# Kernel optimization log

Measured on AMD Instinct MI355X. Metric: run time of the kernel, lower is better.

The kernel has to match this reference:

```python
import jax, jax.numpy as jnp
import numpy as np

N_NODES = 100000
N_EDGES = 1600000
IN_FEATS = 256
HEADS = 4
OUT_FEATS = 32


def setup_inputs() -> dict:
    key = jax.random.key(0)
    k1, k2, k3, k4, k5, k6 = jax.random.split(key, 6)
    feat = jax.random.normal(k1, (N_NODES, IN_FEATS), dtype=jnp.float32)
    fc_w = jax.random.normal(k2, (HEADS * OUT_FEATS, IN_FEATS), dtype=jnp.float32) * (1.0 / np.sqrt(IN_FEATS))
    attn_l = jax.random.normal(k3, (1, HEADS, OUT_FEATS), dtype=jnp.float32) * 0.1
    attn_r = jax.random.normal(k4, (1, HEADS, OUT_FEATS), dtype=jnp.float32) * 0.1
    src = jax.random.randint(k5, (N_EDGES,), 0, N_NODES, dtype=jnp.int32)
    dst = jax.random.randint(k6, (N_EDGES,), 0, N_NODES, dtype=jnp.int32)
    return {"feat": feat, "fc_w": fc_w, "attn_l": attn_l, "attn_r": attn_r, "src": src, "dst": dst}


def reference(feat, fc_w, attn_l, attn_r, src, dst):
    # feat: [N, F_in]; fc_w: [H*D, F_in]; attn_l/r: [1, H, D]; src/dst: [E]
    N = feat.shape[0]
    H, D = attn_l.shape[1], attn_l.shape[2]
    # linear projection (no bias), viewed as [N, H, D]
    ft = (feat @ fc_w.T).reshape(N, H, D)
    # per-node attention logits
    el = jnp.einsum('nhd,hd->nh', ft, attn_l[0])  # [N, H]
    er = jnp.einsum('nhd,hd->nh', ft, attn_r[0])  # [N, H]
    # per-edge score: leaky_relu(el[src] + er[dst])
    e = jax.nn.leaky_relu(el[src] + er[dst], negative_slope=0.2)  # [E, H]
    # edge softmax over incoming edges of each dst node (stable)
    emax = jax.ops.segment_max(e, dst, num_segments=N)  # [N, H]
    a = jnp.exp(e - emax[dst])  # [E, H]
    asum = jax.ops.segment_sum(a, dst, num_segments=N)  # [N, H]
    a = a / asum[dst]
    # attn_drop is a no-op in eval mode; weighted scatter-sum aggregation
    msg = ft[src] * a[:, :, None]  # [E, H, D]
    out = jax.ops.segment_sum(msg, dst, num_segments=N)  # [N, H, D]
    # final_layer=False, activation=None, norm=None -> flatten heads
    return out.reshape(N, H * D)
```

## Files before the change

kernel.cpp:

```cpp
#include <hip/hip_runtime.h>
#include <hip/hip_bf16.h>
#include <float.h>

#define IN_F 256
#define HD   128
#define NH   4
#define GM   128

typedef __bf16 bf16x8 __attribute__((ext_vector_type(8)));
typedef __bf16 bf16x2 __attribute__((ext_vector_type(2)));
typedef float  f32x4  __attribute__((ext_vector_type(4)));

__device__ __forceinline__ bf16x8 cvt8(const float4 a, const float4 b) {
    bf16x8 r;
    r[0] = (__bf16)a.x; r[1] = (__bf16)a.y; r[2] = (__bf16)a.z; r[3] = (__bf16)a.w;
    r[4] = (__bf16)b.x; r[5] = (__bf16)b.y; r[6] = (__bf16)b.z; r[7] = (__bf16)b.w;
    return r;
}

__global__ __launch_bounds__(256) void gemm_ft_mfma(const float* __restrict__ feat,
                                                    const float* __restrict__ w,
                                                    __bf16* __restrict__ ft,
                                                    int N, int ntiles) {
    __shared__ __align__(16) __bf16 Bs[128][264];
    __shared__ __align__(16) __bf16 As[GM][40];
    const int t = threadIdx.x;
    const int wv = t >> 6;
    const int lane = t & 63;

    {
        const int col = t >> 1;
        const int koff = (t & 1) * 128;
        const float* wp = w + (size_t)col * IN_F + koff;
#pragma unroll
        for (int i = 0; i < 128; i += 8) {
            const float4 v0 = *(const float4*)(wp + i);
            const float4 v1 = *(const float4*)(wp + i + 4);
            *(bf16x8*)&Bs[col][koff + i] = cvt8(v0, v1);
        }
    }

    const int ar = t >> 1;
    const int ac = (t & 1) * 16;
    const int frow = lane & 15;
    const int fk   = (lane >> 4) * 8;

    for (int tile = blockIdx.x; tile < ntiles; tile += gridDim.x) {
        const int row0 = tile * GM;
        f32x4 acc[2][8];
#pragma unroll
        for (int mt = 0; mt < 2; ++mt)
#pragma unroll
            for (int ct = 0; ct < 8; ++ct) acc[mt][ct] = {0.f, 0.f, 0.f, 0.f};

        for (int ks = 0; ks < 8; ++ks) {
            const int k0 = ks * 32;
            __syncthreads();
            bf16x8 av0, av1;
            const int gr = row0 + ar;
            if (gr < N) {
                const float* fp = feat + (size_t)gr * IN_F + k0 + ac;
                const float4 v0 = *(const float4*)(fp);
                const float4 v1 = *(const float4*)(fp + 4);
                const float4 v2 = *(const float4*)(fp + 8);
                const float4 v3 = *(const float4*)(fp + 12);
                av0 = cvt8(v0, v1);
                av1 = cvt8(v2, v3);
            } else {
#pragma unroll
                for (int i = 0; i < 8; ++i) { av0[i] = (__bf16)0.f; av1[i] = (__bf16)0.f; }
            }
            *(bf16x8*)&As[ar][ac] = av0;
            *(bf16x8*)&As[ar][ac + 8] = av1;
            __syncthreads();

            const bf16x8 af0 = *(const bf16x8*)&As[wv * 32 + frow][fk];
            const bf16x8 af1 = *(const bf16x8*)&As[wv * 32 + 16 + frow][fk];
#pragma unroll
            for (int ct = 0; ct < 8; ++ct) {
                const bf16x8 bfrag = *(const bf16x8*)&Bs[ct * 16 + frow][k0 + fk];
                acc[0][ct] = __builtin_amdgcn_mfma_f32_16x16x32_bf16(af0, bfrag, acc[0][ct], 0, 0, 0);
                acc[1][ct] = __builtin_amdgcn_mfma_f32_16x16x32_bf16(af1, bfrag, acc[1][ct], 0, 0, 0);
            }
        }
        const int rb = row0 + wv * 32 + (lane >> 4) * 4;
#pragma unroll
        for (int mt = 0; mt < 2; ++mt)
#pragma unroll
            for (int ct = 0; ct < 8; ++ct)
#pragma unroll
                for (int reg = 0; reg < 4; ++reg) {
                    const int m = rb + mt * 16 + reg;
                    if (m < N) ft[(size_t)m * HD + ct * 16 + frow] = (__bf16)acc[mt][ct][reg];
                }
    }
}

__global__ __launch_bounds__(256) void eler_k(const __bf16* __restrict__ ft,
                                              const float* __restrict__ attn_l,
                                              const float* __restrict__ attn_r,
                                              float* __restrict__ el,
                                              float* __restrict__ er, int N) {
    const int lane = threadIdx.x & 63;
    const int node = blockIdx.x * 4 + (threadIdx.x >> 6);
    if (node >= N) return;
    const bf16x2 f  = *(const bf16x2*)(ft + (size_t)node * HD + lane * 2);
    const float2 al = *(const float2*)(attn_l + lane * 2);
    const float2 ar = *(const float2*)(attn_r + lane * 2);
    const float fx = (float)f[0], fy = (float)f[1];
    float pl = fx * al.x + fy * al.y;
    float pr = fx * ar.x + fy * ar.y;
#pragma unroll
    for (int s = 1; s < 16; s <<= 1) {
        pl += __shfl_xor(pl, s);
        pr += __shfl_xor(pr, s);
    }
    if ((lane & 15) == 0) {
        const int h = lane >> 4;
        el[(size_t)node * NH + h] = pl;
        er[(size_t)node * NH + h] = pr;
    }
}

__global__ __launch_bounds__(256) void deg_rank_k(const int* __restrict__ dst,
                                                  int* __restrict__ deg,
                                                  int* __restrict__ rank, int E) {
    const int i = blockIdx.x * 256 + threadIdx.x;
    if (i < E) rank[i] = atomicAdd(&deg[dst[i]], 1);
}

__global__ __launch_bounds__(1024) void scan1_k(const int* __restrict__ deg,
                                                int* __restrict__ off,
                                                int* __restrict__ bsum, int N) {
    __shared__ int lds[1024];
    const int t = threadIdx.x;
    const int g = blockIdx.x * 1024 + t;
    const int x = (g < N) ? deg[g] : 0;
    lds[t] = x;
    __syncthreads();
    int v = x;
    for (int s = 1; s < 1024; s <<= 1) {
        const int add = (t >= s) ? lds[t - s] : 0;
        __syncthreads();
        v += add;
        lds[t] = v;
        __syncthreads();
    }
    if (g < N) off[g] = v - x;
    if (t == 1023) bsum[blockIdx.x] = v;
}

__global__ __launch_bounds__(128) void scan2_k(const int* __restrict__ bsum,
                                               int* __restrict__ boff, int nb) {
    __shared__ int lds[128];
    const int t = threadIdx.x;
    const int x = (t < nb) ? bsum[t] : 0;
    lds[t] = x;
    __syncthreads();
    int v = x;
    for (int s = 1; s < 128; s <<= 1) {
        const int add = (t >= s) ? lds[t - s] : 0;
        __syncthreads();
        v += add;
        lds[t] = v;
        __syncthreads();
    }
    boff[t] = v - x;
}

__global__ __launch_bounds__(256) void scatter_k(const int* __restrict__ src,
                                                 const int* __restrict__ dst,
                                                 const int* __restrict__ off,
                                                 const int* __restrict__ boff,
                                                 const int* __restrict__ rank,
                                                 int* __restrict__ ssrc, int E) {
    const int i = blockIdx.x * 256 + threadIdx.x;
    if (i < E) {
        const int d = dst[i];
        const int p = off[d] + boff[d >> 10] + rank[i];
        ssrc[p] = src[i];
    }
}

__global__ __launch_bounds__(64) void aggregate_k(const __bf16* __restrict__ ft,
                                                  const float* __restrict__ el,
                                                  const float* __restrict__ er,
                                                  const int* __restrict__ deg,
                                                  const int* __restrict__ off,
                                                  const int* __restrict__ boff,
                                                  const int* __restrict__ ssrc,
                                                  float* __restrict__ out, int N) {
    const int n = blockIdx.x;
    const int lane = threadIdx.x;
    const int il = lane & 15;
    const int q  = lane >> 4;
    const int h  = il >> 2;
    float4* outp = (float4*)(out + (size_t)n * HD);
    const int dn = deg[n];
    if (dn == 0) {
        if (q < 2) outp[il * 2 + q] = make_float4(0.f, 0.f, 0.f, 0.f);
        return;
    }
    const int start = off[n] + boff[n >> 10];
    const float4 er4 = *(const float4*)(er + (size_t)n * NH);

    __shared__ float a_lds[64 * NH];
    __shared__ int   s_lds[64];
    float4 ssum = make_float4(0.f, 0.f, 0.f, 0.f);
    float acc[8];
#pragma unroll
    for (int i = 0; i < 8; ++i) acc[i] = 0.f;

    for (int c0 = 0; c0 < dn; c0 += 64) {
        const int j = c0 + lane;
        float4 a = make_float4(0.f, 0.f, 0.f, 0.f);
        int sv = 0;
        if (j < dn) {
            sv = ssrc[start + j];
            float4 e = *(const float4*)(el + (size_t)sv * NH);
            e.x += er4.x; e.y += er4.y; e.z += er4.z; e.w += er4.w;
            e.x = e.x >= 0.f ? e.x : 0.2f * e.x;
            e.y = e.y >= 0.f ? e.y : 0.2f * e.y;
            e.z = e.z >= 0.f ? e.z : 0.2f * e.z;
            e.w = e.w >= 0.f ? e.w : 0.2f * e.w;
            a.x = __expf(e.x); a.y = __expf(e.y);
            a.z = __expf(e.z); a.w = __expf(e.w);
            ssum.x += a.x; ssum.y += a.y; ssum.z += a.z; ssum.w += a.w;
        }
        s_lds[lane] = sv;
        *(float4*)(a_lds + lane * NH) = a;
        __syncthreads();
        const int cnt = min(64, dn - c0);
        for (int j2 = 0; j2 < cnt; j2 += 8) {
            const int e0 = j2 + q;
            const int e1 = j2 + 4 + q;
            const int sv0 = s_lds[e0];
            const int sv1 = s_lds[e1];
            const float a0 = a_lds[e0 * NH + h];
            const float a1 = a_lds[e1 * NH + h];
            const bf16x8 f0 = *(const bf16x8*)(ft + (size_t)sv0 * HD + il * 8);
            const bf16x8 f1 = *(const bf16x8*)(ft + (size_t)sv1 * HD + il * 8);
#pragma unroll
            for (int k = 0; k < 8; ++k) acc[k] = fmaf(a0, (float)f0[k], acc[k]);
#pragma unroll
            for (int k = 0; k < 8; ++k) acc[k] = fmaf(a1, (float)f1[k], acc[k]);
        }
        __syncthreads();
    }
#pragma unroll
    for (int s = 1; s < 64; s <<= 1) {
        ssum.x += __shfl_xor(ssum.x, s);
        ssum.y += __shfl_xor(ssum.y, s);
        ssum.z += __shfl_xor(ssum.z, s);
        ssum.w += __shfl_xor(ssum.w, s);
    }
#pragma unroll
    for (int k = 0; k < 8; ++k) {
        acc[k] += __shfl_xor(acc[k], 16);
        acc[k] += __shfl_xor(acc[k], 32);
    }
    const float sumh = (h == 0) ? ssum.x : (h == 1) ? ssum.y : (h == 2) ? ssum.z : ssum.w;
    const float inv = 1.f / sumh;
    if (q < 2) {
        const int b = q * 4;
        outp[il * 2 + q] = make_float4(acc[b] * inv, acc[b + 1] * inv,
                                       acc[b + 2] * inv, acc[b + 3] * inv);
    }
}

extern "C" void kernel_launch(void* const* d_in, const int* in_sizes, int n_in,
                              void* d_out, int out_size, void* d_ws, size_t ws_size,
                              hipStream_t stream) {
    const float* feat   = (const float*)d_in[0];
    const float* fc_w   = (const float*)d_in[1];
    const float* attn_l = (const float*)d_in[2];
    const float* attn_r = (const float*)d_in[3];
    const int*   src    = (const int*)d_in[4];
    const int*   dst    = (const int*)d_in[5];
    const int N = in_sizes[0] / IN_F;
    const int E = in_sizes[4];
    float* out = (float*)d_out;

    char* wp = (char*)d_ws;
    __bf16* ft = (__bf16*)wp; wp += (size_t)N * HD * 2;
    float* el  = (float*)wp; wp += (size_t)N * NH * 4;
    float* er  = (float*)wp; wp += (size_t)N * NH * 4;
    int* deg   = (int*)wp;   wp += (size_t)N * 4;
    int* off   = (int*)wp;   wp += (size_t)N * 4;
    int* bsum  = (int*)wp;   wp += 1024;
    int* boff  = (int*)wp;   wp += 1024;
    int* rank  = (int*)wp;   wp += (size_t)E * 4;
    int* ssrc  = (int*)wp;   wp += (size_t)E * 4;

    hipMemsetAsync(deg, 0, (size_t)N * 4, stream);

    const int ntiles = (N + GM - 1) / GM;
    gemm_ft_mfma<<<dim3(512), dim3(256), 0, stream>>>(feat, fc_w, ft, N, ntiles);
    eler_k<<<dim3((N + 3) / 4), dim3(256), 0, stream>>>(ft, attn_l, attn_r, el, er, N);
    deg_rank_k<<<dim3((E + 255) / 256), dim3(256), 0, stream>>>(dst, deg, rank, E);
    const int nblk = (N + 1023) >> 10;
    scan1_k<<<dim3(nblk), dim3(1024), 0, stream>>>(deg, off, bsum, N);
    scan2_k<<<dim3(1), dim3(128), 0, stream>>>(bsum, boff, nblk);
    scatter_k<<<dim3((E + 255) / 256), dim3(256), 0, stream>>>(src, dst, off, boff, rank, ssrc, E);
    aggregate_k<<<dim3(N), dim3(64), 0, stream>>>(ft, el, er, deg, off, boff, ssrc, out, N);
}
```

Measured before the change: 386.9 us.

## Fuse el/er logits and degree counting into GEMM with register prefetch

Merges the projection GEMM, the per-node attention logit computation and the destination degree/rank atomic counting into one kernel, which removes two launches and the re-read of ft. el/er are now computed from the fp32 MFMA accumulators using cross-lane shuffles instead of from the bf16-rounded ft. The feat tile for the next k-step is also prefetched into registers so that global loads overlap the MFMA work. In exchange the kernel uses more registers and its GEMM phase is delayed by the atomic loop, and el/er now differ slightly numerically from the bf16 path.

```diff
diff --git a/kernel.cpp b/kernel.cpp
--- a/kernel.cpp
+++ b/kernel.cpp
@@ -18,10 +18,17 @@
     return r;
 }
 
-__global__ __launch_bounds__(256) void gemm_ft_mfma(const float* __restrict__ feat,
-                                                    const float* __restrict__ w,
-                                                    __bf16* __restrict__ ft,
-                                                    int N, int ntiles) {
+__global__ __launch_bounds__(256) void gemm_fused(const float* __restrict__ feat,
+                                                  const float* __restrict__ w,
+                                                  const float* __restrict__ attn_l,
+                                                  const float* __restrict__ attn_r,
+                                                  const int* __restrict__ dst,
+                                                  __bf16* __restrict__ ft,
+                                                  float* __restrict__ el,
+                                                  float* __restrict__ er,
+                                                  int* __restrict__ deg,
+                                                  int* __restrict__ rank,
+                                                  int N, int E, int ntiles) {
     __shared__ __align__(16) __bf16 Bs[128][264];
     __shared__ __align__(16) __bf16 As[GM][40];
     const int t = threadIdx.x;
@@ -40,10 +47,35 @@
         }
     }
 
-    const int ar = t >> 1;
-    const int ac = (t & 1) * 16;
+    for (int i = blockIdx.x * 256 + t; i < E; i += gridDim.x * 256)
+        rank[i] = atomicAdd(&deg[dst[i]], 1);
+
     const int frow = lane & 15;
     const int fk   = (lane >> 4) * 8;
+
+    float alw[8], arw[8];
+#pragma unroll
+    for (int ct = 0; ct < 8; ++ct) {
+        alw[ct] = attn_l[ct * 16 + frow];
+        arw[ct] = attn_r[ct * 16 + frow];
+    }
+
+    const int ar_ = t >> 1;
+    const int ac  = (t & 1) * 16;
+
+    float4 p0, p1, p2, p3;
+    {
+        const int gr = blockIdx.x * GM + ar_;
+        if (gr < N) {
+            const float* fp = feat + (size_t)gr * IN_F + ac;
+            p0 = *(const float4*)(fp);
+            p1 = *(const float4*)(fp + 4);
+            p2 = *(const float4*)(fp + 8);
+            p3 = *(const float4*)(fp + 12);
+        } else {
+            p0 = p1 = p2 = p3 = make_float4(0.f, 0.f, 0.f, 0.f);
+        }
+    }
 
     for (int tile = blockIdx.x; tile < ntiles; tile += gridDim.x) {
         const int row0 = tile * GM;
@@ -54,26 +86,27 @@
             for (int ct = 0; ct < 8; ++ct) acc[mt][ct] = {0.f, 0.f, 0.f, 0.f};
 
         for (int ks = 0; ks < 8; ++ks) {
+            __syncthreads();
+            *(bf16x8*)&As[ar_][ac]     = cvt8(p0, p1);
+            *(bf16x8*)&As[ar_][ac + 8] = cvt8(p2, p3);
+
+            const int ntile = (ks < 7) ? tile : tile + gridDim.x;
+            const int nks   = (ks < 7) ? ks + 1 : 0;
+            if (ntile < ntiles) {
+                const int gr = ntile * GM + ar_;
+                if (gr < N) {
+                    const float* fp = feat + (size_t)gr * IN_F + nks * 32 + ac;
+                    p0 = *(const float4*)(fp);
+                    p1 = *(const float4*)(fp + 4);
+                    p2 = *(const float4*)(fp + 8);
+                    p3 = *(const float4*)(fp + 12);
+                } else {
+                    p0 = p1 = p2 = p3 = make_float4(0.f, 0.f, 0.f, 0.f);
+                }
+            }
+
+            __syncthreads();
             const int k0 = ks * 32;
-            __syncthreads();
-            bf16x8 av0, av1;
-            const int gr = row0 + ar;
-            if (gr < N) {
-                const float* fp = feat + (size_t)gr * IN_F + k0 + ac;
-                const float4 v0 = *(const float4*)(fp);
-                const float4 v1 = *(const float4*)(fp + 4);
-                const float4 v2 = *(const float4*)(fp + 8);
-                const float4 v3 = *(const float4*)(fp + 12);
-                av0 = cvt8(v0, v1);
-                av1 = cvt8(v2, v3);
-            } else {
-#pragma unroll
-                for (int i = 0; i < 8; ++i) { av0[i] = (__bf16)0.f; av1[i] = (__bf16)0.f; }
-            }
-            *(bf16x8*)&As[ar][ac] = av0;
-            *(bf16x8*)&As[ar][ac + 8] = av1;
-            __syncthreads();
-
             const bf16x8 af0 = *(const bf16x8*)&As[wv * 32 + frow][fk];
             const bf16x8 af1 = *(const bf16x8*)&As[wv * 32 + 16 + frow][fk];
 #pragma unroll
@@ -83,50 +116,60 @@
                 acc[1][ct] = __builtin_amdgcn_mfma_f32_16x16x32_bf16(af1, bfrag, acc[1][ct], 0, 0, 0);
             }
         }
+
         const int rb = row0 + wv * 32 + (lane >> 4) * 4;
-#pragma unroll
-        for (int mt = 0; mt < 2; ++mt)
-#pragma unroll
-            for (int ct = 0; ct < 8; ++ct)
-#pragma unroll
-                for (int reg = 0; reg < 4; ++reg) {
-                    const int m = rb + mt * 16 + reg;
-                    if (m < N) ft[(size_t)m * HD + ct * 16 + frow] = (__bf16)acc[mt][ct][reg];
+        if (row0 + GM <= N) {
+#pragma unroll
+            for (int mt = 0; mt < 2; ++mt)
+#pragma unroll
+                for (int ct = 0; ct < 8; ++ct)
+#pragma unroll
+                    for (int reg = 0; reg < 4; ++reg) {
+                        const int m = rb + mt * 16 + reg;
+                        ft[(size_t)m * HD + ct * 16 + frow] = (__bf16)acc[mt][ct][reg];
+                    }
+        } else {
+#pragma unroll
+            for (int mt = 0; mt < 2; ++mt)
+#pragma unroll
+                for (int ct = 0; ct < 8; ++ct)
+#pragma unroll
+                    for (int reg = 0; reg < 4; ++reg) {
+                        const int m = rb + mt * 16 + reg;
+                        if (m < N) ft[(size_t)m * HD + ct * 16 + frow] = (__bf16)acc[mt][ct][reg];
+                    }
+        }
+
+#pragma unroll
+        for (int mt = 0; mt < 2; ++mt) {
+#pragma unroll
+            for (int reg = 0; reg < 4; ++reg) {
+                float pl[4], pr[4];
+#pragma unroll
+                for (int h = 0; h < 4; ++h) {
+                    const float v0 = acc[mt][2 * h][reg];
+                    const float v1 = acc[mt][2 * h + 1][reg];
+                    pl[h] = v0 * alw[2 * h] + v1 * alw[2 * h + 1];
+                    pr[h] = v0 * arw[2 * h] + v1 * arw[2 * h + 1];
                 }
-    }
-}
-
-__global__ __launch_bounds__(256) void eler_k(const __bf16* __restrict__ ft,
-                                              const float* __restrict__ attn_l,
-                                              const float* __restrict__ attn_r,
-                                              float* __restrict__ el,
-                                              float* __restrict__ er, int N) {
-    const int lane = threadIdx.x & 63;
-    const int node = blockIdx.x * 4 + (threadIdx.x >> 6);
-    if (node >= N) return;
-    const bf16x2 f  = *(const bf16x2*)(ft + (size_t)node * HD + lane * 2);
-    const float2 al = *(const float2*)(attn_l + lane * 2);
-    const float2 ar = *(const float2*)(attn_r + lane * 2);
-    const float fx = (float)f[0], fy = (float)f[1];
-    float pl = fx * al.x + fy * al.y;
-    float pr = fx * ar.x + fy * ar.y;
-#pragma unroll
-    for (int s = 1; s < 16; s <<= 1) {
-        pl += __shfl_xor(pl, s);
-        pr += __shfl_xor(pr, s);
-    }
-    if ((lane & 15) == 0) {
-        const int h = lane >> 4;
-        el[(size_t)node * NH + h] = pl;
-        er[(size_t)node * NH + h] = pr;
-    }
-}
-
-__global__ __launch_bounds__(256) void deg_rank_k(const int* __restrict__ dst,
-                                                  int* __restrict__ deg,
-                                                  int* __restrict__ rank, int E) {
-    const int i = blockIdx.x * 256 + threadIdx.x;
-    if (i < E) rank[i] = atomicAdd(&deg[dst[i]], 1);
+#pragma unroll
+                for (int s = 1; s < 16; s <<= 1) {
+#pragma unroll
+                    for (int h = 0; h < 4; ++h) {
+                        pl[h] += __shfl_xor(pl[h], s);
+                        pr[h] += __shfl_xor(pr[h], s);
+                    }
+                }
+                if (frow == 0) {
+                    const int r = row0 + wv * 32 + mt * 16 + (lane >> 4) * 4 + reg;
+                    if (r < N) {
+                        *(float4*)(el + (size_t)r * NH) = make_float4(pl[0], pl[1], pl[2], pl[3]);
+                        *(float4*)(er + (size_t)r * NH) = make_float4(pr[0], pr[1], pr[2], pr[3]);
+                    }
+                }
+            }
+        }
+    }
 }
 
 __global__ __launch_bounds__(1024) void scan1_k(const int* __restrict__ deg,
@@ -295,9 +338,8 @@
     hipMemsetAsync(deg, 0, (size_t)N * 4, stream);
 
     const int ntiles = (N + GM - 1) / GM;
-    gemm_ft_mfma<<<dim3(512), dim3(256), 0, stream>>>(feat, fc_w, ft, N, ntiles);
-    eler_k<<<dim3((N + 3) / 4), dim3(256), 0, stream>>>(ft, attn_l, attn_r, el, er, N);
-    deg_rank_k<<<dim3((E + 255) / 256), dim3(256), 0, stream>>>(dst, deg, rank, E);
+    gemm_fused<<<dim3(512), dim3(256), 0, stream>>>(feat, fc_w, attn_l, attn_r, dst,
+                                                    ft, el, er, deg, rank, N, E, ntiles);
     const int nblk = (N + 1023) >> 10;
     scan1_k<<<dim3(nblk), dim3(1024), 0, stream>>>(deg, off, bsum, N);
     scan2_k<<<dim3(1), dim3(128), 0, stream>>>(bsum, boff, nblk);
```

New measurement: 364.6 us. -5.8%, faster.
